# Kernel optimization log

Measured on AMD Instinct MI355X. Metric: run time of the kernel, lower is better.

The kernel has to match this reference:

```python
import jax, jax.numpy as jnp
import numpy as np

# Faithful JAX version of ROIMask_To_Img / paste_mask_in_image (Mask R-CNN paste):
# per box: (mask+1)/2, zero-pad by 1, expand box by (M+2)/M, truncate to int,
# bilinear-resize (align_corners=False, edge-clamped) to the box extent, and
# overwrite-paste into the image canvas; final canvas is mapped to [-1, 1].
# Instead of per-box dynamic-size interpolate + slice assignment, we evaluate the
# bilinear resample densely over the full image grid and mask to the box region
# (same math, jit-compatible, single fused gather-resize-scatter).


def _edge_coords(s, size):
    # torch bilinear align_corners=False with edge clamping
    s = jnp.clip(s, 0.0, size - 1.0)
    i0 = jnp.floor(s)
    t = s - i0
    i0 = i0.astype(jnp.int32)
    i1 = jnp.minimum(i0 + 1, size - 1)
    return i0, i1, t


def _paste_step(im, mask, box):
    # im: [H, W] canvas; mask: [M, M] in [-1,1]; box: [4] float (x0, y0, x1, y1)
    H, W = im.shape
    M = mask.shape[-1]
    Mp = M + 2  # padded mask size
    m = jnp.pad((mask + 1.0) * 0.5, 1)  # expand_masks(padding=1) -> [Mp, Mp]
    scale = (M + 2.0) / M
    w_half = (box[2] - box[0]) * (0.5 * scale)
    h_half = (box[3] - box[1]) * (0.5 * scale)
    x_c = (box[2] + box[0]) * 0.5
    y_c = (box[3] + box[1]) * 0.5
    # expand_boxes then .to(int32) (truncation toward zero, like torch)
    b = jnp.trunc(jnp.stack([x_c - w_half, y_c - h_half,
                             x_c + w_half, y_c + h_half])).astype(jnp.int32)
    w = jnp.maximum(b[2] - b[0] + 1, 1).astype(jnp.float32)
    h = jnp.maximum(b[3] - b[1] + 1, 1).astype(jnp.float32)
    px = jnp.arange(H)
    py = jnp.arange(W)
    # source coords in padded-mask space (align_corners=False)
    sx = (px - b[0] + 0.5) * (Mp / w) - 0.5  # [H]
    sy = (py - b[1] + 0.5) * (Mp / h) - 0.5  # [W]
    x0, x1, tx = _edge_coords(sx, Mp)
    y0, y1, ty = _edge_coords(sy, Mp)
    # separable bilinear: mix rows first ([H, Mp]), then columns ([H, W])
    rowmix = m[x0] * (1.0 - tx)[:, None] + m[x1] * tx[:, None]
    val = rowmix[:, y0] * (1.0 - ty)[None, :] + rowmix[:, y1] * ty[None, :]
    # paste region (overwrite semantics, clipped to the image)
    vx = (px >= b[0]) & (px <= b[2])
    vy = (py >= b[1]) & (py <= b[3])
    return jnp.where(vx[:, None] & vy[None, :], val, im)


def setup_inputs() -> dict:
    key = jax.random.key(0)
    B, N, M, H, W = 32, 16, 28, 1024, 1024
    k1, k2, k3, k4 = jax.random.split(key, 4)
    masks = jax.random.uniform(k1, (B, N, 1, M, M), jnp.float32, -1.0, 1.0)
    # valid boxes inside the image: corner + extent
    p0 = jax.random.uniform(k2, (B, N, 2), jnp.float32, 0.0, H - 64.0)
    ext = jax.random.uniform(k3, (B, N, 2), jnp.float32, 16.0, 200.0)
    p1 = jnp.minimum(p0 + ext, H - 2.0)
    rects = jnp.concatenate([p0, p1], axis=-1)  # [B, N, 4] = (x0, y0, x1, y1)
    instance_mask = jnp.zeros((B, 1, H, W), jnp.float32)
    return {"masks": masks, "rects": rects, "instance_mask": instance_mask}


def reference(masks, rects, instance_mask):
    # masks: [B, N, 1, M, M]; rects: [B, N, 4]; instance_mask: [B, 1, H, W]
    H, W = instance_mask.shape[-2], instance_mask.shape[-1]

    def per_image(masks_b, rects_b):
        im0 = jnp.zeros((H, W), jnp.float32)
        def step(im, xs):
            m, bx = xs
            return _paste_step(im, m, bx), None
        im, _ = jax.lax.scan(step, im0, (masks_b[:, 0], rects_b))
        return im

    im = jax.vmap(per_image)(masks, rects)  # [B, H, W]
    return im[:, None, :, :] * 2.0 - 1.0
```

## Files before the change

### kernel.cpp

```cpp
#include <hip/hip_runtime.h>

constexpr int Bc  = 32;
constexpr int Nc  = 16;
constexpr int Mc  = 28;
constexpr int MPc = 30;
constexpr int Hc  = 1024;
constexpr int Wc  = 1024;
constexpr int NBOX = Bc * Nc;
constexpr int CHROWS = 16;
constexpr int MAXCH  = 14;

__global__ __launch_bounds__(256)
void fill_kernel(float4* __restrict__ out)
{
    const float4 v = make_float4(-1.0f, -1.0f, -1.0f, -1.0f);
    const size_t base = (size_t)blockIdx.x * 1024 + threadIdx.x;
    out[base]       = v;
    out[base + 256] = v;
    out[base + 512] = v;
    out[base + 768] = v;
}

__global__ __launch_bounds__(256)
void paste_boxes_kernel(const float* __restrict__ masks,
                        const float* __restrict__ rects,
                        float* __restrict__ out)
{
    const int box = blockIdx.x;
    const int b   = box >> 4;
    const int n   = box & (Nc - 1);
    const int tid = threadIdx.x;

    __shared__ int4 s_rect[Nc];
    __shared__ int4 s_row[CHROWS];

    if (tid < Nc) {
        const float* r = rects + (b * Nc + tid) * 4;
        const float x0 = r[0], y0 = r[1], x1 = r[2], y1 = r[3];
        const float hs = 0.5357142857142857f;
        const float w_half = (x1 - x0) * hs;
        const float h_half = (y1 - y0) * hs;
        const float xc = (x1 + x0) * 0.5f;
        const float yc = (y1 + y0) * 0.5f;
        s_rect[tid] = make_int4((int)truncf(xc - w_half),
                                (int)truncf(yc - h_half),
                                (int)truncf(xc + w_half),
                                (int)truncf(yc + h_half));
    }
    __syncthreads();

    const int4 rc  = s_rect[n];
    const int  rlo = max(rc.x, 0);
    const int  rhi = min(rc.z, Hc - 1);
    const int  r0  = rlo + (int)blockIdx.y * CHROWS;
    if (r0 > rhi) return;
    const int r1 = min(r0 + CHROWS - 1, rhi);

    const float w   = fmaxf((float)(rc.z - rc.x + 1), 1.0f);
    const float h   = fmaxf((float)(rc.w - rc.y + 1), 1.0f);
    const float scx = (float)MPc / w;
    const float scy = (float)MPc / h;

    if (tid < CHROWS) {
        const int row = r0 + tid;
        unsigned m = 0;
        #pragma unroll
        for (int k = 0; k < Nc; ++k)
            if (row >= s_rect[k].x && row <= s_rect[k].z) m |= (1u << k);
        float sx = ((float)(row - rc.x) + 0.5f) * scx - 0.5f;
        sx = fminf(fmaxf(sx, 0.0f), (float)(MPc - 1));
        const int   i0 = (int)floorf(sx);
        const float tx = sx - (float)i0;
        const int   i1 = min(i0 + 1, MPc - 1);
        s_row[tid] = make_int4(i0, i1, __float_as_int(tx), (int)m);
    }

    const int clo = max(rc.y, 0);
    const int col = clo + tid;
    unsigned cmask = 0;
    if (col < Wc) {
        #pragma unroll
        for (int k = 0; k < Nc; ++k)
            if (col >= s_rect[k].y && col <= s_rect[k].w) cmask |= (1u << k);
    }
    float sy = ((float)(col - rc.y) + 0.5f) * scy - 0.5f;
    sy = fminf(fmaxf(sy, 0.0f), (float)(MPc - 1));
    const int   j0 = (int)floorf(sy);
    const float ty = sy - (float)j0;
    const int   j1 = min(j0 + 1, MPc - 1);
    const bool jok0 = (j0 >= 1) & (j0 <= Mc);
    const bool jok1 = (j1 >= 1) & (j1 <= Mc);
    const float* mp = masks + (size_t)box * (Mc * Mc);
    __syncthreads();

    float* oimg = out + (size_t)b * Hc * Wc;

    for (int rr = 0; rr <= r1 - r0; ++rr) {
        const int4 rd = s_row[rr];
        const unsigned m = cmask & (unsigned)rd.w;
        if ((m >> n) == 1u) {
            const int   i0 = rd.x, i1 = rd.y;
            const float tx = __int_as_float(rd.z);
            const bool iok0 = (i0 >= 1) & (i0 <= Mc);
            const bool iok1 = (i1 >= 1) & (i1 <= Mc);
            const float m00 = (iok0 & jok0) ? (mp[(i0-1)*Mc + (j0-1)] + 1.0f) * 0.5f : 0.0f;
            const float m10 = (iok1 & jok0) ? (mp[(i1-1)*Mc + (j0-1)] + 1.0f) * 0.5f : 0.0f;
            const float m01 = (iok0 & jok1) ? (mp[(i0-1)*Mc + (j1-1)] + 1.0f) * 0.5f : 0.0f;
            const float m11 = (iok1 & jok1) ? (mp[(i1-1)*Mc + (j1-1)] + 1.0f) * 0.5f : 0.0f;
            const float a0 = m00 * (1.0f - tx) + m10 * tx;
            const float a1 = m01 * (1.0f - tx) + m11 * tx;
            const float val = (a0 * (1.0f - ty) + a1 * ty) * 2.0f - 1.0f;
            oimg[(size_t)(r0 + rr) * Wc + col] = val;
        }
    }
}

extern "C" void kernel_launch(void* const* d_in, const int* in_sizes, int n_in,
                              void* d_out, int out_size, void* d_ws, size_t ws_size,
                              hipStream_t stream) {
    const float* masks = (const float*)d_in[0];
    const float* rects = (const float*)d_in[1];
    float* out = (float*)d_out;

    const int n4 = out_size / 4;
    const int fill_grid = n4 / 1024;
    fill_kernel<<<fill_grid, 256, 0, stream>>>((float4*)out);

    dim3 grid2(NBOX, MAXCH);
    paste_boxes_kernel<<<grid2, 256, 0, stream>>>(masks, rects, out);
}
```

Measured before the change: 246.7 us.

## Precompute box rects and row/column coverage masks in a prep kernel

Adds a per-image prep kernel that computes the expanded integer rects, scale factors and 16-bit row/column coverage bitmasks once, storing them in workspace. The paste kernel now loads these instead of recomputing the rects and running 16-way overlap loops in every block. Row chunks are doubled to 32 rows with half as many chunks per box. This adds one small kernel launch and a dependency on workspace layout in exchange for less redundant per-block setup work.

```diff
diff --git a/kernel.cpp b/kernel.cpp
--- a/kernel.cpp
+++ b/kernel.cpp
@@ -6,9 +6,56 @@
 constexpr int MPc = 30;
 constexpr int Hc  = 1024;
 constexpr int Wc  = 1024;
-constexpr int NBOX = Bc * Nc;
-constexpr int CHROWS = 16;
-constexpr int MAXCH  = 14;
+constexpr int NBOX   = Bc * Nc;
+constexpr int CHROWS = 32;
+constexpr int MAXCH  = 7;
+
+
+__global__ __launch_bounds__(256)
+void prep_kernel(const float* __restrict__ rects,
+                 int4* __restrict__ rectbuf,
+                 float2* __restrict__ scalebuf,
+                 unsigned short* __restrict__ rowmaskbuf,
+                 unsigned short* __restrict__ colmaskbuf)
+{
+    const int b   = blockIdx.x;
+    const int tid = threadIdx.x;
+    __shared__ int4 s_rect[Nc];
+
+    if (tid < Nc) {
+        const float* r = rects + (b * Nc + tid) * 4;
+        const float x0 = r[0], y0 = r[1], x1 = r[2], y1 = r[3];
+        const float hs = 0.5357142857142857f;
+        const float w_half = (x1 - x0) * hs;
+        const float h_half = (y1 - y0) * hs;
+        const float xc = (x1 + x0) * 0.5f;
+        const float yc = (y1 + y0) * 0.5f;
+        const int4 rc = make_int4((int)truncf(xc - w_half),
+                                  (int)truncf(yc - h_half),
+                                  (int)truncf(xc + w_half),
+                                  (int)truncf(yc + h_half));
+        s_rect[tid] = rc;
+        rectbuf[b * Nc + tid] = rc;
+        const float w = fmaxf((float)(rc.z - rc.x + 1), 1.0f);
+        const float h = fmaxf((float)(rc.w - rc.y + 1), 1.0f);
+        scalebuf[b * Nc + tid] = make_float2((float)MPc / w, (float)MPc / h);
+    }
+    __syncthreads();
+
+    #pragma unroll
+    for (int i = 0; i < 4; ++i) {
+        const int pos = tid + i * 256;
+        unsigned rm = 0, cm = 0;
+        #pragma unroll
+        for (int k = 0; k < Nc; ++k) {
+            const int4 rc = s_rect[k];
+            if (pos >= rc.x && pos <= rc.z) rm |= (1u << k);
+            if (pos >= rc.y && pos <= rc.w) cm |= (1u << k);
+        }
+        rowmaskbuf[b * Hc + pos] = (unsigned short)rm;
+        colmaskbuf[b * Wc + pos] = (unsigned short)cm;
+    }
+}
 
 __global__ __launch_bounds__(256)
 void fill_kernel(float4* __restrict__ out)
@@ -23,7 +70,10 @@
 
 __global__ __launch_bounds__(256)
 void paste_boxes_kernel(const float* __restrict__ masks,
-                        const float* __restrict__ rects,
+                        const int4* __restrict__ rectbuf,
+                        const float2* __restrict__ scalebuf,
+                        const unsigned short* __restrict__ rowmaskbuf,
+                        const unsigned short* __restrict__ colmaskbuf,
                         float* __restrict__ out)
 {
     const int box = blockIdx.x;
@@ -31,59 +81,34 @@
     const int n   = box & (Nc - 1);
     const int tid = threadIdx.x;
 
-    __shared__ int4 s_rect[Nc];
-    __shared__ int4 s_row[CHROWS];
-
-    if (tid < Nc) {
-        const float* r = rects + (b * Nc + tid) * 4;
-        const float x0 = r[0], y0 = r[1], x1 = r[2], y1 = r[3];
-        const float hs = 0.5357142857142857f;
-        const float w_half = (x1 - x0) * hs;
-        const float h_half = (y1 - y0) * hs;
-        const float xc = (x1 + x0) * 0.5f;
-        const float yc = (y1 + y0) * 0.5f;
-        s_rect[tid] = make_int4((int)truncf(xc - w_half),
-                                (int)truncf(yc - h_half),
-                                (int)truncf(xc + w_half),
-                                (int)truncf(yc + h_half));
-    }
-    __syncthreads();
-
-    const int4 rc  = s_rect[n];
+    const int4 rc  = rectbuf[box];
     const int  rlo = max(rc.x, 0);
     const int  rhi = min(rc.z, Hc - 1);
     const int  r0  = rlo + (int)blockIdx.y * CHROWS;
     if (r0 > rhi) return;
-    const int r1 = min(r0 + CHROWS - 1, rhi);
+    const int  r1  = min(r0 + CHROWS - 1, rhi);
+    const float2 sc = scalebuf[box];
 
-    const float w   = fmaxf((float)(rc.z - rc.x + 1), 1.0f);
-    const float h   = fmaxf((float)(rc.w - rc.y + 1), 1.0f);
-    const float scx = (float)MPc / w;
-    const float scy = (float)MPc / h;
+    __shared__ int4 s_row[CHROWS];
 
     if (tid < CHROWS) {
         const int row = r0 + tid;
-        unsigned m = 0;
-        #pragma unroll
-        for (int k = 0; k < Nc; ++k)
-            if (row >= s_rect[k].x && row <= s_rect[k].z) m |= (1u << k);
-        float sx = ((float)(row - rc.x) + 0.5f) * scx - 0.5f;
+        const unsigned rm = (row <= rhi) ? rowmaskbuf[b * Hc + row] : 0u;
+        float sx = ((float)(row - rc.x) + 0.5f) * sc.x - 0.5f;
         sx = fminf(fmaxf(sx, 0.0f), (float)(MPc - 1));
         const int   i0 = (int)floorf(sx);
         const float tx = sx - (float)i0;
         const int   i1 = min(i0 + 1, MPc - 1);
-        s_row[tid] = make_int4(i0, i1, __float_as_int(tx), (int)m);
+        s_row[tid] = make_int4(i0, i1, __float_as_int(tx), (int)rm);
     }
 
     const int clo = max(rc.y, 0);
+    const int chi = min(rc.w, Wc - 1);
     const int col = clo + tid;
-    unsigned cmask = 0;
-    if (col < Wc) {
-        #pragma unroll
-        for (int k = 0; k < Nc; ++k)
-            if (col >= s_rect[k].y && col <= s_rect[k].w) cmask |= (1u << k);
-    }
-    float sy = ((float)(col - rc.y) + 0.5f) * scy - 0.5f;
+    const bool colok = (col <= chi);
+    const unsigned cmask = colok ? (unsigned)colmaskbuf[b * Wc + col] : 0u;
+
+    float sy = ((float)(col - rc.y) + 0.5f) * sc.y - 0.5f;
     sy = fminf(fmaxf(sy, 0.0f), (float)(MPc - 1));
     const int   j0 = (int)floorf(sy);
     const float ty = sy - (float)j0;
@@ -94,8 +119,9 @@
     __syncthreads();
 
     float* oimg = out + (size_t)b * Hc * Wc;
+    const int nr = r1 - r0;
 
-    for (int rr = 0; rr <= r1 - r0; ++rr) {
+    for (int rr = 0; rr <= nr; ++rr) {
         const int4 rd = s_row[rr];
         const unsigned m = cmask & (unsigned)rd.w;
         if ((m >> n) == 1u) {
@@ -122,10 +148,18 @@
     const float* rects = (const float*)d_in[1];
     float* out = (float*)d_out;
 
+    int4*           rectbuf  = (int4*)d_ws;
+    float2*         scalebuf = (float2*)((char*)d_ws + 8192);
+    unsigned short* rowmaskb = (unsigned short*)((char*)d_ws + 12288);
+    unsigned short* colmaskb = (unsigned short*)((char*)d_ws + 77824);
+
+    prep_kernel<<<Bc, 256, 0, stream>>>(rects, rectbuf, scalebuf,
+                                        rowmaskb, colmaskb);
+
     const int n4 = out_size / 4;
-    const int fill_grid = n4 / 1024;
-    fill_kernel<<<fill_grid, 256, 0, stream>>>((float4*)out);
+    fill_kernel<<<n4 / 1024, 256, 0, stream>>>((float4*)out);
 
     dim3 grid2(NBOX, MAXCH);
-    paste_boxes_kernel<<<grid2, 256, 0, stream>>>(masks, rects, out);
+    paste_boxes_kernel<<<grid2, 256, 0, stream>>>(masks, rectbuf, scalebuf,
+                                                  rowmaskb, colmaskb, out);
 }
```

New measurement: 257.8 us. 1.04x slower.
